# Kernel tuning notes

Hardware: AMD Instinct MI355X
Metric: run time of the kernel (lower is better)

## Reference

```python
import jax, jax.numpy as jnp
import numpy as np

B, S, D_IN, D_OUT, H = 4, 2048, 1024, 1024, 16
HD = D_OUT // H  # head_dim = 64


def setup_inputs() -> dict:
    key = jax.random.key(0)
    ks = jax.random.split(key, 9)
    sc_in = 1.0 / np.sqrt(D_IN)
    sc_out = 1.0 / np.sqrt(D_OUT)
    return {
        "x": jax.random.normal(ks[0], (B, S, D_IN), dtype=jnp.float32),
        "Wq": jax.random.normal(ks[1], (D_IN, D_OUT), dtype=jnp.float32) * sc_in,
        "bq": jax.random.normal(ks[2], (D_OUT,), dtype=jnp.float32) * 0.01,
        "Wk": jax.random.normal(ks[3], (D_IN, D_OUT), dtype=jnp.float32) * sc_in,
        "bk": jax.random.normal(ks[4], (D_OUT,), dtype=jnp.float32) * 0.01,
        "Wv": jax.random.normal(ks[5], (D_IN, D_OUT), dtype=jnp.float32) * sc_in,
        "bv": jax.random.normal(ks[6], (D_OUT,), dtype=jnp.float32) * 0.01,
        "Wo": jax.random.normal(ks[7], (D_OUT, D_OUT), dtype=jnp.float32) * sc_out,
        "bo": jax.random.normal(ks[8], (D_OUT,), dtype=jnp.float32) * 0.01,
    }


def reference(x, Wq, bq, Wk, bk, Wv, bv, Wo, bo):
    b, s, _ = x.shape
    # QKV projections -> [b, h, s, hd]
    def proj(W, bias):
        return (x @ W + bias).reshape(b, s, H, HD).transpose(0, 2, 1, 3)
    q, k, v = proj(Wq, bq), proj(Wk, bk), proj(Wv, bv)
    # scaled scores [b, h, s, s] with causal mask (future positions -> -inf)
    scores = jnp.einsum("bhqd,bhkd->bhqk", q, k) / jnp.sqrt(jnp.float32(HD))
    causal = jnp.triu(jnp.ones((s, s), dtype=bool), k=1)
    scores = jnp.where(causal, -jnp.inf, scores)
    attn = jax.nn.softmax(scores, axis=-1)  # dropout p=0.0 -> identity
    ctx = jnp.einsum("bhqk,bhkd->bhqd", attn, v)
    ctx = ctx.transpose(0, 2, 1, 3).reshape(b, s, D_OUT)
    return ctx @ Wo + bo
```

## Files before the change

### kernel.cpp

```cpp
#include <hip/hip_runtime.h>
#include <hip/hip_bf16.h>

#define B_   4
#define S_   2048
#define H_   16
#define HD_  64
#define D_   1024
#define M_   (B_ * S_)
#define N3_  3072

typedef unsigned short u16;
typedef __bf16 bf16x8 __attribute__((ext_vector_type(8)));
typedef float  f32x4  __attribute__((ext_vector_type(4)));
typedef int    i32x4  __attribute__((ext_vector_type(4)));
typedef unsigned short u16x8 __attribute__((ext_vector_type(8)));
typedef unsigned short u16x4 __attribute__((ext_vector_type(4)));

__device__ __forceinline__ float b2f(u16 u) {
    unsigned int x = ((unsigned int)u) << 16;
    return __builtin_bit_cast(float, x);
}
__device__ __forceinline__ u16 f2b(float f) {
    unsigned int x = __builtin_bit_cast(unsigned int, f);
    x += 0x7fffu + ((x >> 16) & 1u);
    return (u16)(x >> 16);
}

typedef const __attribute__((address_space(1))) unsigned int* gas_u32p;
typedef __attribute__((address_space(3))) unsigned int* las_u32p;
__device__ __forceinline__ void gl_lds16(const u16* g, u16* lds_base) {
    __builtin_amdgcn_global_load_lds((gas_u32p)g, (las_u32p)lds_base, 16, 0, 0);
}

__global__ __launch_bounds__(256) void cvt_k(const float* __restrict__ in,
                                             u16* __restrict__ out) {
    size_t i = ((size_t)blockIdx.x * 256 + threadIdx.x) * 8;
    float4 a = *(const float4*)(in + i);
    float4 b = *(const float4*)(in + i + 4);
    *(u16x8*)(out + i) = u16x8{f2b(a.x), f2b(a.y), f2b(a.z), f2b(a.w),
                               f2b(b.x), f2b(b.y), f2b(b.z), f2b(b.w)};
}

__global__ __launch_bounds__(256) void transpose4_k(
    const float* __restrict__ w0, const float* __restrict__ w1,
    const float* __restrict__ w2, const float* __restrict__ w3,
    u16* __restrict__ oqkv, u16* __restrict__ owo, float scale0) {
    __shared__ u16 t[32][33];
    const int z = blockIdx.z;
    const float* in = (z == 0) ? w0 : (z == 1) ? w1 : (z == 2) ? w2 : w3;
    u16* out = (z < 3) ? oqkv + (size_t)z * D_ * D_ : owo;
    const float sc = (z == 0) ? scale0 : 1.0f;
    const int x0 = blockIdx.x * 32, y0 = blockIdx.y * 32;
    const int tx = threadIdx.x & 31, ty = threadIdx.x >> 5;
#pragma unroll
    for (int i = 0; i < 32; i += 8)
        t[ty + i][tx] = f2b(in[(size_t)(y0 + ty + i) * D_ + x0 + tx] * sc);
    __syncthreads();
#pragma unroll
    for (int i = 0; i < 32; i += 8)
        out[(size_t)(x0 + ty + i) * D_ + y0 + tx] = t[tx][ty + i];
}

#define QBM 256
#define QBN 192
#define QBK 64

__global__ __launch_bounds__(512, 2) void gemm_qkv256(
    const u16* __restrict__ A, const u16* __restrict__ Bt,
    const float* __restrict__ b0, const float* __restrict__ b1,
    const float* __restrict__ b2, float cscale,
    u16* __restrict__ Qo, u16* __restrict__ Ko, u16* __restrict__ Vto,
    int M, int N, int K)
{
    __shared__ __align__(16) u16 As[2][QBM * QBK];
    __shared__ __align__(16) u16 Bs[2][QBN * QBK];

    const int tid  = threadIdx.x;
    const int lane = tid & 63;
    const int wave = tid >> 6;
    const int wr = wave >> 2, wc = wave & 3;
    const int l15 = lane & 15, quad = lane >> 4, s7 = l15 & 7;
    const int r8  = lane >> 3;
    const int csw = ((lane & 7) ^ r8) * 8;
    const int m0 = blockIdx.x * QBM, n0 = blockIdx.y * QBN;
    (void)M; (void)N;

    const u16* Ag = A  + (size_t)(m0 + wave * 8 + r8) * K + csw;
    const u16* Bg = Bt + (size_t)(n0 + wave * 8 + r8) * K + csw;
    u16* AsW = &As[0][0] + wave * 8 * QBK;
    u16* BsW = &Bs[0][0] + wave * 8 * QBK;
    const size_t rowK64 = (size_t)64 * K;

    auto stgA = [&](int buf, int u, int kt) {
        gl_lds16(Ag + (size_t)u * rowK64 + kt * QBK,
                 AsW + buf * (QBM * QBK) + u * 64 * QBK);
    };
    auto stgB = [&](int buf, int u, int kt) {
        gl_lds16(Bg + (size_t)u * rowK64 + kt * QBK,
                 BsW + buf * (QBN * QBK) + u * 64 * QBK);
    };

    f32x4 acc[8][3] = {};

    stgA(0, 0, 0); stgA(0, 1, 0); stgA(0, 2, 0); stgA(0, 3, 0);
    stgB(0, 0, 0); stgB(0, 1, 0); stgB(0, 2, 0);
    stgB(1, 0, 1); stgB(1, 1, 1); stgB(1, 2, 1);
    asm volatile("s_waitcnt vmcnt(3)" ::: "memory");
    __builtin_amdgcn_s_barrier();

    const int NIT = K / (2 * QBK);
    for (int it = 0; it < NIT; ++it) {
        const bool last = (it == NIT - 1);
        const int t1 = 2 * it + 1, t2 = 2 * it + 2, t3 = 2 * it + 3;
        bf16x8 bn[3][2];
#pragma unroll
        for (int ph = 0; ph < 4; ++ph) {
            const int hb = ph >> 1;
            const int qg = ph & 1;
            const u16* as = &As[hb][0];
            const u16* bs = &Bs[hb][0];
            if (qg == 0) {
#pragma unroll
                for (int n = 0; n < 3; ++n) {
                    const u16* bp = bs + (wc * 48 + n * 16 + l15) * QBK;
                    bn[n][0] = *(const bf16x8*)(bp + ((quad    ) ^ s7) * 8);
                    bn[n][1] = *(const bf16x8*)(bp + ((quad + 4) ^ s7) * 8);
                }
            }
            bf16x8 af[4][2];
#pragma unroll
            for (int r = 0; r < 4; ++r) {
                const u16* ap = as + (wr * 128 + (qg * 4 + r) * 16 + l15) * QBK;
                af[r][0] = *(const bf16x8*)(ap + ((quad    ) ^ s7) * 8);
                af[r][1] = *(const bf16x8*)(ap + ((quad + 4) ^ s7) * 8);
            }
            if (ph == 0) { stgA(1, 0, t1); stgA(1, 1, t1);
                           stgA(1, 2, t1); stgA(1, 3, t1); }
            if (!last) {
                if (ph == 1) { stgB(0, 0, t2); stgB(0, 1, t2); stgB(0, 2, t2); }
                if (ph == 2) { stgA(0, 0, t2); stgA(0, 1, t2);
                               stgA(0, 2, t2); stgA(0, 3, t2); }
                if (ph == 3) { stgB(1, 0, t3); stgB(1, 1, t3); stgB(1, 2, t3); }
            }
            __builtin_amdgcn_s_barrier();
            asm volatile("s_waitcnt lgkmcnt(0)" ::: "memory");
            __builtin_amdgcn_sched_barrier(0);
            __builtin_amdgcn_s_setprio(1);
#pragma unroll
            for (int r = 0; r < 4; ++r)
#pragma unroll
                for (int n = 0; n < 3; ++n) {
                    acc[qg * 4 + r][n] = __builtin_amdgcn_mfma_f32_16x16x32_bf16(
                        af[r][0], bn[n][0], acc[qg * 4 + r][n], 0, 0, 0);
                    acc[qg * 4 + r][n] = __builtin_amdgcn_mfma_f32_16x16x32_bf16(
                        af[r][1], bn[n][1], acc[qg * 4 + r][n], 0, 0, 0);
                }
            __builtin_amdgcn_s_setprio(0);
            if (ph == 1) {
                if (!last) asm volatile("s_waitcnt vmcnt(3)" ::: "memory");
                else       asm volatile("s_waitcnt vmcnt(0)" ::: "memory");
            }
            if (ph == 3 && !last)
                asm volatile("s_waitcnt vmcnt(3)" ::: "memory");
            __builtin_amdgcn_s_barrier();
        }
    }

    int qidxv[3]; int ncolv[3]; float bvv[3];
#pragma unroll
    for (int nt = 0; nt < 3; ++nt) {
        const int col = n0 + wc * 48 + nt * 16 + l15;
        qidxv[nt] = col >> 10;
        ncolv[nt] = col & (D_ - 1);
        bvv[nt] = (qidxv[nt] == 0) ? b0[ncolv[nt]] * cscale
                : (qidxv[nt] == 1) ? b1[ncolv[nt]] : b2[ncolv[nt]];
    }
#pragma unroll
    for (int mt = 0; mt < 8; ++mt) {
        const int rbase = m0 + wr * 128 + mt * 16 + quad * 4;
#pragma unroll
        for (int r2 = 0; r2 < 4; ++r2) {
#pragma unroll
            for (int nt = 0; nt < 3; ++nt) {
                if (qidxv[nt] == 2) continue;
                u16* dst = (qidxv[nt] == 0) ? Qo : Ko;
                dst[(size_t)(rbase + r2) * D_ + ncolv[nt]] =
                    f2b(acc[mt][nt][r2] + bvv[nt]);
            }
        }
#pragma unroll
        for (int nt = 0; nt < 3; ++nt) {
            if (qidxv[nt] != 2) continue;
            const int bidx = rbase >> 11, s = rbase & (S_ - 1);
            const int hh = ncolv[nt] >> 6, hd = ncolv[nt] & 63;
            u16x4 pk{f2b(acc[mt][nt][0] + bvv[nt]), f2b(acc[mt][nt][1] + bvv[nt]),
                     f2b(acc[mt][nt][2] + bvv[nt]), f2b(acc[mt][nt][3] + bvv[nt])};
            *(u16x4*)(Vto + (((size_t)(bidx * H_ + hh)) * HD_ + hd) * S_ + s) = pk;
        }
    }
}

#define BM 128
#define BN 128
#define BK 64

template <int MODE>
__global__ __launch_bounds__(256) void gemm_core(
    const u16* __restrict__ A, const u16* __restrict__ Bt,
    const float* __restrict__ b0, const float* __restrict__ b1,
    const float* __restrict__ b2, float cscale,
    void* __restrict__ O0, void* __restrict__ O1, void* __restrict__ O2,
    int M, int N, int K)
{
    __shared__ __align__(16) u16 As[BM * BK];
    __shared__ __align__(16) u16 Bs[BN * BK];

    const int tid  = threadIdx.x;
    const int lane = tid & 63;
    const int wave = tid >> 6;
    const int wr = wave >> 1, wc = wave & 1;
    const int l15 = lane & 15, quad = lane >> 4;
    const int m0 = blockIdx.x * BM, n0 = blockIdx.y * BN;
    const int r8 = lane >> 3;
    const int csw = ((lane & 7) ^ r8) * 8;

    f32x4 acc[4][4] = {};

    for (int k0 = 0; k0 < K; k0 += BK) {
#pragma unroll
        for (int i = 0; i < 4; ++i) {
            const int row = wave * 32 + i * 8 + r8;
            gl_lds16(A  + (size_t)(m0 + row) * K + k0 + csw,
                     As + (wave * 32 + i * 8) * BK);
            gl_lds16(Bt + (size_t)(n0 + row) * K + k0 + csw,
                     Bs + (wave * 32 + i * 8) * BK);
        }
        __syncthreads();
        bf16x8 af[4][2], bfr[4][2];
#pragma unroll
        for (int t = 0; t < 4; ++t) {
            const u16* ap = As + (wr * 64 + t * 16 + l15) * BK;
            const u16* bp = Bs + (wc * 64 + t * 16 + l15) * BK;
            const int s7 = l15 & 7;
            af[t][0]  = *(const bf16x8*)(ap + ((quad    ) ^ s7) * 8);
            af[t][1]  = *(const bf16x8*)(ap + ((quad + 4) ^ s7) * 8);
            bfr[t][0] = *(const bf16x8*)(bp + ((quad    ) ^ s7) * 8);
            bfr[t][1] = *(const bf16x8*)(bp + ((quad + 4) ^ s7) * 8);
        }
#pragma unroll
        for (int mt = 0; mt < 4; ++mt)
#pragma unroll
            for (int nt = 0; nt < 4; ++nt) {
                acc[mt][nt] = __builtin_amdgcn_mfma_f32_16x16x32_bf16(
                    af[mt][0], bfr[nt][0], acc[mt][nt], 0, 0, 0);
                acc[mt][nt] = __builtin_amdgcn_mfma_f32_16x16x32_bf16(
                    af[mt][1], bfr[nt][1], acc[mt][nt], 0, 0, 0);
            }
        __syncthreads();
    }

#pragma unroll
    for (int nt = 0; nt < 4; ++nt) {
        const int col = n0 + wc * 64 + nt * 16 + l15;
        if constexpr (MODE == 1) {
            const float bv = b0[col];
#pragma unroll
            for (int mt = 0; mt < 4; ++mt) {
                const int rbase = m0 + wr * 64 + mt * 16 + quad * 4;
#pragma unroll
                for (int r2 = 0; r2 < 4; ++r2)
                    ((float*)O0)[(size_t)(rbase + r2) * N + col] =
                        acc[mt][nt][r2] + bv;
            }
        } else {
            const int qidx = col >> 10, ncol = col & (D_ - 1);
            const float bv = (qidx == 0) ? b0[ncol] * cscale
                           : (qidx == 1) ? b1[ncol] : b2[ncol];
#pragma unroll
            for (int mt = 0; mt < 4; ++mt) {
                const int rbase = m0 + wr * 64 + mt * 16 + quad * 4;
                if (qidx == 2) {
                    const int bidx = rbase >> 11, s = rbase & (S_ - 1);
                    const int hh = ncol >> 6, hd = ncol & 63;
                    u16x4 pk{f2b(acc[mt][nt][0] + bv), f2b(acc[mt][nt][1] + bv),
                             f2b(acc[mt][nt][2] + bv), f2b(acc[mt][nt][3] + bv)};
                    *(u16x4*)((u16*)O2 +
                        (((size_t)(bidx * H_ + hh)) * HD_ + hd) * S_ + s) = pk;
                } else {
                    u16* dst = (qidx == 0) ? (u16*)O0 : (u16*)O1;
#pragma unroll
                    for (int r2 = 0; r2 < 4; ++r2)
                        dst[(size_t)(rbase + r2) * D_ + ncol] =
                            f2b(acc[mt][nt][r2] + bv);
                }
            }
        }
    }
}

__global__ __launch_bounds__(256, 4) void attn_mfma_k(
    const u16* __restrict__ Qm, const u16* __restrict__ Km,
    const u16* __restrict__ Vtg, u16* __restrict__ Om)
{
    __shared__ __align__(16) u16 Kbuf[2][64 * 64];
    __shared__ __align__(16) u16 Vbuf[2][64 * 64];
    __shared__ __align__(16) u16 Ps[4][16 * 64];

    const int tid  = threadIdx.x;
    const int lane = tid & 63;
    const int wave = tid >> 6;
    const int l15  = lane & 15;
    const int quad = lane >> 4;
    const int s7   = l15 & 7;
    const int bh = blockIdx.x, b = bh >> 4, h = bh & (H_ - 1);
    const int j  = blockIdx.y;
    const int dg0 = j, dg1 = 31 - j;

    const u16* Qg = Qm + (size_t)b * S_ * D_ + h * HD_;
    const u16* Kg = Km + (size_t)b * S_ * D_ + h * HD_;
    const u16* Vg = Vtg + ((size_t)(b * H_ + h)) * HD_ * S_;

    bf16x8 qf0[2], qf1[2];
    {
        const u16* qp = Qg + (size_t)(dg0 * 64 + wave * 16 + l15) * D_ + quad * 8;
        qf0[0] = *(const bf16x8*)qp; qf0[1] = *(const bf16x8*)(qp + 32);
        qp = Qg + (size_t)(dg1 * 64 + wave * 16 + l15) * D_ + quad * 8;
        qf1[0] = *(const bf16x8*)qp; qf1[1] = *(const bf16x8*)(qp + 32);
    }

    f32x4 of0[4] = {}, of1[4] = {};
    float lacc0 = 0.f, lacc1 = 0.f;
    const int qloc = wave * 16 + l15;
    const int r8 = lane >> 3;
    const int csw = ((lane & 7) ^ r8) * 8;
    const int srcA = l15 + ((quad & 1) << 5);
    const int srcB = srcA + 16;

    auto stage = [&](int t, int bsel) {
        u16* kb = Kbuf[bsel];
        u16* vb = Vbuf[bsel];
#pragma unroll
        for (int i = 0; i < 2; ++i) {
            const int row = wave * 16 + i * 8 + r8;
            gl_lds16(Kg + (size_t)(t * 64 + row) * D_ + csw,
                     kb + (wave * 16 + i * 8) * 64);
            gl_lds16(Vg + (size_t)row * S_ + t * 64 + csw,
                     vb + (wave * 16 + i * 8) * 64);
        }
    };

    auto pass = [&](const bf16x8 (&q)[2], f32x4 (&o)[4], float& la,
                    bool domask, const u16* kb, const u16* vb) {
        f32x4 sf[4];
#pragma unroll
        for (int kt = 0; kt < 4; ++kt) {
            const u16* kp = kb + (kt * 16 + l15) * 64;
            bf16x8 k0 = *(const bf16x8*)(kp + ((quad    ) ^ s7) * 8);
            bf16x8 k1 = *(const bf16x8*)(kp + ((quad + 4) ^ s7) * 8);
            f32x4 a = {};
            a = __builtin_amdgcn_mfma_f32_16x16x32_bf16(k0, q[0], a, 0, 0, 0);
            a = __builtin_amdgcn_mfma_f32_16x16x32_bf16(k1, q[1], a, 0, 0, 0);
            sf[kt] = a;
        }
        unsigned int w[4][2];
        float ls = 0.f;
        if (domask) {
#pragma unroll
            for (int kt = 0; kt < 4; ++kt)
#pragma unroll
                for (int hh = 0; hh < 2; ++hh) {
                    float v0 = sf[kt][2 * hh], v1 = sf[kt][2 * hh + 1];
                    if (kt * 16 + quad * 4 + 2 * hh     > qloc) v0 = -INFINITY;
                    if (kt * 16 + quad * 4 + 2 * hh + 1 > qloc) v1 = -INFINITY;
                    float p0 = __builtin_amdgcn_exp2f(v0);
                    float p1 = __builtin_amdgcn_exp2f(v1);
                    ls += p0 + p1;
                    w[kt][hh] = (__builtin_bit_cast(unsigned int, p0) >> 16) |
                                (__builtin_bit_cast(unsigned int, p1) & 0xFFFF0000u);
                }
        } else {
#pragma unroll
            for (int kt = 0; kt < 4; ++kt)
#pragma unroll
                for (int hh = 0; hh < 2; ++hh) {
                    float p0 = __builtin_amdgcn_exp2f(sf[kt][2 * hh]);
                    float p1 = __builtin_amdgcn_exp2f(sf[kt][2 * hh + 1]);
                    ls += p0 + p1;
                    w[kt][hh] = (__builtin_bit_cast(unsigned int, p0) >> 16) |
                                (__builtin_bit_cast(unsigned int, p1) & 0xFFFF0000u);
                }
        }
        la += ls;
        const bool hi = (quad & 2) != 0;
        i32x4 f0, f1;
        {
            int a0, a1;
            a0 = __shfl((int)w[0][0], srcA); a1 = __shfl((int)w[1][0], srcA);
            f0.x = hi ? a1 : a0;
            a0 = __shfl((int)w[0][1], srcA); a1 = __shfl((int)w[1][1], srcA);
            f0.y = hi ? a1 : a0;
            a0 = __shfl((int)w[0][0], srcB); a1 = __shfl((int)w[1][0], srcB);
            f0.z = hi ? a1 : a0;
            a0 = __shfl((int)w[0][1], srcB); a1 = __shfl((int)w[1][1], srcB);
            f0.w = hi ? a1 : a0;
            a0 = __shfl((int)w[2][0], srcA); a1 = __shfl((int)w[3][0], srcA);
            f1.x = hi ? a1 : a0;
            a0 = __shfl((int)w[2][1], srcA); a1 = __shfl((int)w[3][1], srcA);
            f1.y = hi ? a1 : a0;
            a0 = __shfl((int)w[2][0], srcB); a1 = __shfl((int)w[3][0], srcB);
            f1.z = hi ? a1 : a0;
            a0 = __shfl((int)w[2][1], srcB); a1 = __shfl((int)w[3][1], srcB);
            f1.w = hi ? a1 : a0;
        }
        bf16x8 pf0 = __builtin_bit_cast(bf16x8, f0);
        bf16x8 pf1 = __builtin_bit_cast(bf16x8, f1);
#pragma unroll
        for (int dt = 0; dt < 4; ++dt) {
            const u16* vp = vb + (dt * 16 + l15) * 64;
            bf16x8 v0 = *(const bf16x8*)(vp + ((quad    ) ^ s7) * 8);
            bf16x8 v1 = *(const bf16x8*)(vp + ((quad + 4) ^ s7) * 8);
            o[dt] = __builtin_amdgcn_mfma_f32_16x16x32_bf16(v0, pf0, o[dt], 0, 0, 0);
            o[dt] = __builtin_amdgcn_mfma_f32_16x16x32_bf16(v1, pf1, o[dt], 0, 0, 0);
        }
    };

    const int T = 32 - j;
    stage(0, 0);
    for (int t = 0; t < T; ++t) {
        __syncthreads();
        if (t + 1 < T) stage(t + 1, (t + 1) & 1);
        const u16* kb = Kbuf[t & 1];
        const u16* vb = Vbuf[t & 1];
        if (t <= dg0) pass(qf0, of0, lacc0, t == dg0, kb, vb);
        pass(qf1, of1, lacc1, t == dg1, kb, vb);
    }

    u16* pw = Ps[wave];
    auto epi = [&](const f32x4 (&o)[4], float la, int dgq) {
        float ls = la;
        ls += __shfl_xor(ls, 16);
        ls += __shfl_xor(ls, 32);
        const float inv = 1.f / ls;
#pragma unroll
        for (int dt = 0; dt < 4; ++dt) {
            const int g = dt * 16 + quad * 4;
            const int pos = ((g >> 3) ^ s7) * 8 + (g & 7);
            *(u16x4*)(pw + l15 * 64 + pos) =
                u16x4{f2b(o[dt][0] * inv), f2b(o[dt][1] * inv),
                      f2b(o[dt][2] * inv), f2b(o[dt][3] * inv)};
        }
        const int r  = lane >> 2;
        const int cp = lane & 3;
        u16x8 o0 = *(const u16x8*)(pw + r * 64 + ((2 * cp    ) ^ (r & 7)) * 8);
        u16x8 o1 = *(const u16x8*)(pw + r * 64 + ((2 * cp + 1) ^ (r & 7)) * 8);
        u16* op = Om + ((size_t)(b * S_ + dgq * 64 + wave * 16 + r)) * D_ + h * 64 + cp * 16;
        *(u16x8*)op = o0;
        *(u16x8*)(op + 8) = o1;
    };
    epi(of0, lacc0, dg0);
    epi(of1, lacc1, dg1);
}

extern "C" void kernel_launch(void* const* d_in, const int* in_sizes, int n_in,
                              void* d_out, int out_size, void* d_ws, size_t ws_size,
                              hipStream_t stream)
{
    (void)in_sizes; (void)n_in; (void)out_size; (void)ws_size;
    const float* x  = (const float*)d_in[0];
    const float* Wq = (const float*)d_in[1];
    const float* bq = (const float*)d_in[2];
    const float* Wk = (const float*)d_in[3];
    const float* bk = (const float*)d_in[4];
    const float* Wv = (const float*)d_in[5];
    const float* bv = (const float*)d_in[6];
    const float* Wo = (const float*)d_in[7];
    const float* bo = (const float*)d_in[8];

    const float cscale = 0.18033688011112042f;

    u16* ws = (u16*)d_ws;
    const size_t MD = (size_t)M_ * D_;
    const size_t DD = (size_t)D_ * D_;
    u16* xb    = ws;
    u16* Qb    = xb + MD;
    u16* Kb    = Qb + MD;
    u16* Vtb   = Kb + MD;
    u16* Cb    = Vtb + MD;
    u16* WqkvT = Cb + MD;
    u16* WoT   = WqkvT + 3 * DD;

    cvt_k<<<M_ * D_ / 2048, 256, 0, stream>>>(x, xb);

    transpose4_k<<<dim3(D_ / 32, D_ / 32, 4), 256, 0, stream>>>(
        Wq, Wk, Wv, Wo, WqkvT, WoT, cscale);

    gemm_qkv256<<<dim3(M_ / QBM, N3_ / QBN), 512, 0, stream>>>(
        xb, WqkvT, bq, bk, bv, cscale, Qb, Kb, Vtb, M_, N3_, D_);

    attn_mfma_k<<<dim3(B_ * H_, 16), 256, 0, stream>>>(Qb, Kb, Vtb, Cb);

    gemm_core<1><<<dim3(M_ / BM, D_ / BN), 256, 0, stream>>>(
        Cb, WoT, bo, nullptr, nullptr, 1.0f, d_out, nullptr, nullptr, M_, D_, D_);
}
```

Before: 264.8 us.

## Interleave both query tiles' QK and PV MFMAs sharing K/V LDS loads, add setprio

Splits the per-tile attention pass into score, softmax and PV phases and runs the two query fragments together, so each K and V fragment read from LDS feeds MFMAs for both query tiles. Interleaving independent MFMA chains is meant to hide MFMA latency and halve LDS reads for K/V. s_setprio raises wave priority around the MFMA phases to encourage overlap with other waves' softmax. This raises register pressure by holding two score sets live at once.

```diff
diff --git a/kernel.cpp b/kernel.cpp
--- a/kernel.cpp
+++ b/kernel.cpp
@@ -349,19 +349,8 @@
         }
     };
 
-    auto pass = [&](const bf16x8 (&q)[2], f32x4 (&o)[4], float& la,
-                    bool domask, const u16* kb, const u16* vb) {
-        f32x4 sf[4];
-#pragma unroll
-        for (int kt = 0; kt < 4; ++kt) {
-            const u16* kp = kb + (kt * 16 + l15) * 64;
-            bf16x8 k0 = *(const bf16x8*)(kp + ((quad    ) ^ s7) * 8);
-            bf16x8 k1 = *(const bf16x8*)(kp + ((quad + 4) ^ s7) * 8);
-            f32x4 a = {};
-            a = __builtin_amdgcn_mfma_f32_16x16x32_bf16(k0, q[0], a, 0, 0, 0);
-            a = __builtin_amdgcn_mfma_f32_16x16x32_bf16(k1, q[1], a, 0, 0, 0);
-            sf[kt] = a;
-        }
+    auto smax = [&](const f32x4 (&sf)[4], bool domask, float& la,
+                    bf16x8& pfa, bf16x8& pfb) {
         unsigned int w[4][2];
         float ls = 0.f;
         if (domask) {
@@ -412,16 +401,8 @@
             a0 = __shfl((int)w[2][1], srcB); a1 = __shfl((int)w[3][1], srcB);
             f1.w = hi ? a1 : a0;
         }
-        bf16x8 pf0 = __builtin_bit_cast(bf16x8, f0);
-        bf16x8 pf1 = __builtin_bit_cast(bf16x8, f1);
-#pragma unroll
-        for (int dt = 0; dt < 4; ++dt) {
-            const u16* vp = vb + (dt * 16 + l15) * 64;
-            bf16x8 v0 = *(const bf16x8*)(vp + ((quad    ) ^ s7) * 8);
-            bf16x8 v1 = *(const bf16x8*)(vp + ((quad + 4) ^ s7) * 8);
-            o[dt] = __builtin_amdgcn_mfma_f32_16x16x32_bf16(v0, pf0, o[dt], 0, 0, 0);
-            o[dt] = __builtin_amdgcn_mfma_f32_16x16x32_bf16(v1, pf1, o[dt], 0, 0, 0);
-        }
+        pfa = __builtin_bit_cast(bf16x8, f0);
+        pfb = __builtin_bit_cast(bf16x8, f1);
     };
 
     const int T = 32 - j;
@@ -431,8 +412,67 @@
         if (t + 1 < T) stage(t + 1, (t + 1) & 1);
         const u16* kb = Kbuf[t & 1];
         const u16* vb = Vbuf[t & 1];
-        if (t <= dg0) pass(qf0, of0, lacc0, t == dg0, kb, vb);
-        pass(qf1, of1, lacc1, t == dg1, kb, vb);
+
+        if (t <= dg0) {
+            f32x4 s0[4], s1[4];
+            __builtin_amdgcn_s_setprio(1);
+#pragma unroll
+            for (int kt = 0; kt < 4; ++kt) {
+                const u16* kp = kb + (kt * 16 + l15) * 64;
+                bf16x8 k0 = *(const bf16x8*)(kp + ((quad    ) ^ s7) * 8);
+                bf16x8 k1 = *(const bf16x8*)(kp + ((quad + 4) ^ s7) * 8);
+                f32x4 a = {};
+                a = __builtin_amdgcn_mfma_f32_16x16x32_bf16(k0, qf0[0], a, 0, 0, 0);
+                a = __builtin_amdgcn_mfma_f32_16x16x32_bf16(k1, qf0[1], a, 0, 0, 0);
+                s0[kt] = a;
+                f32x4 c = {};
+                c = __builtin_amdgcn_mfma_f32_16x16x32_bf16(k0, qf1[0], c, 0, 0, 0);
+                c = __builtin_amdgcn_mfma_f32_16x16x32_bf16(k1, qf1[1], c, 0, 0, 0);
+                s1[kt] = c;
+            }
+            __builtin_amdgcn_s_setprio(0);
+            bf16x8 p00, p01, p10, p11;
+            smax(s0, t == dg0, lacc0, p00, p01);
+            smax(s1, false,    lacc1, p10, p11);
+            __builtin_amdgcn_s_setprio(1);
+#pragma unroll
+            for (int dt = 0; dt < 4; ++dt) {
+                const u16* vp = vb + (dt * 16 + l15) * 64;
+                bf16x8 v0 = *(const bf16x8*)(vp + ((quad    ) ^ s7) * 8);
+                bf16x8 v1 = *(const bf16x8*)(vp + ((quad + 4) ^ s7) * 8);
+                of0[dt] = __builtin_amdgcn_mfma_f32_16x16x32_bf16(v0, p00, of0[dt], 0, 0, 0);
+                of0[dt] = __builtin_amdgcn_mfma_f32_16x16x32_bf16(v1, p01, of0[dt], 0, 0, 0);
+                of1[dt] = __builtin_amdgcn_mfma_f32_16x16x32_bf16(v0, p10, of1[dt], 0, 0, 0);
+                of1[dt] = __builtin_amdgcn_mfma_f32_16x16x32_bf16(v1, p11, of1[dt], 0, 0, 0);
+            }
+            __builtin_amdgcn_s_setprio(0);
+        } else {
+            f32x4 s1[4];
+            __builtin_amdgcn_s_setprio(1);
+#pragma unroll
+            for (int kt = 0; kt < 4; ++kt) {
+                const u16* kp = kb + (kt * 16 + l15) * 64;
+                bf16x8 k0 = *(const bf16x8*)(kp + ((quad    ) ^ s7) * 8);
+                bf16x8 k1 = *(const bf16x8*)(kp + ((quad + 4) ^ s7) * 8);
+                f32x4 c = {};
+                c = __builtin_amdgcn_mfma_f32_16x16x32_bf16(k0, qf1[0], c, 0, 0, 0);
+                c = __builtin_amdgcn_mfma_f32_16x16x32_bf16(k1, qf1[1], c, 0, 0, 0);
+                s1[kt] = c;
+            }
+            __builtin_amdgcn_s_setprio(0);
+            bf16x8 p10, p11;
+            smax(s1, t == dg1, lacc1, p10, p11);
+            __builtin_amdgcn_s_setprio(1);
+#pragma unroll
+            for (int dt = 0; dt < 4; ++dt) {
+                const u16* vp = vb + (dt * 16 + l15) * 64;
+                bf16x8 v0 = *(const bf16x8*)(vp + ((quad    ) ^ s7) * 8);
+                bf16x8 v1 = *(const bf16x8*)(vp + ((quad + 4) ^ s7) * 8);
+                of1[dt] = __builtin_amdgcn_mfma_f32_16x16x32_bf16(v0, p10, of1[dt], 0, 0, 0);
+                of1[dt] = __builtin_amdgcn_mfma_f32_16x16x32_bf16(v1, p11, of1[dt], 0, 0, 0);
+            }
+            __builtin_amdgcn_s_setprio(0);
+        }
     }
 
     u16* pw = Ps[wave];
```

After: 284.3 us. 1.07x slower.

## Read K and V tiles directly from global memory instead of LDS staging

Applied to the files above, without the earlier changes.

Drops the double-buffered global-to-LDS staging of K and V tiles, along with the per-iteration __syncthreads, in the causal attention kernel. Each wave now loads its MFMA operands straight from global memory, relying on L1/L2 caching across the four waves that read the same tile. This removes the barriers and the LDS traffic, but it multiplies global and cache load requests by the wave count and loses the prefetch overlap. Any latency hiding now depends on the compiler's scheduling and on occupancy.

```diff
diff --git a/kernel.cpp b/kernel.cpp
--- a/kernel.cpp
+++ b/kernel.cpp
@@ -302,8 +302,6 @@
     const u16* __restrict__ Qm, const u16* __restrict__ Km,
     const u16* __restrict__ Vtg, u16* __restrict__ Om)
 {
-    __shared__ __align__(16) u16 Kbuf[2][64 * 64];
-    __shared__ __align__(16) u16 Vbuf[2][64 * 64];
     __shared__ __align__(16) u16 Ps[4][16 * 64];
 
     const int tid  = threadIdx.x;
@@ -331,32 +329,18 @@
     f32x4 of0[4] = {}, of1[4] = {};
     float lacc0 = 0.f, lacc1 = 0.f;
     const int qloc = wave * 16 + l15;
-    const int r8 = lane >> 3;
-    const int csw = ((lane & 7) ^ r8) * 8;
     const int srcA = l15 + ((quad & 1) << 5);
     const int srcB = srcA + 16;
 
-    auto stage = [&](int t, int bsel) {
-        u16* kb = Kbuf[bsel];
-        u16* vb = Vbuf[bsel];
-#pragma unroll
-        for (int i = 0; i < 2; ++i) {
-            const int row = wave * 16 + i * 8 + r8;
-            gl_lds16(Kg + (size_t)(t * 64 + row) * D_ + csw,
-                     kb + (wave * 16 + i * 8) * 64);
-            gl_lds16(Vg + (size_t)row * S_ + t * 64 + csw,
-                     vb + (wave * 16 + i * 8) * 64);
-        }
-    };
-
     auto pass = [&](const bf16x8 (&q)[2], f32x4 (&o)[4], float& la,
-                    bool domask, const u16* kb, const u16* vb) {
+                    bool domask, int t) {
         f32x4 sf[4];
+        const u16* kp0 = Kg + (size_t)(t * 64 + l15) * D_ + quad * 8;
 #pragma unroll
         for (int kt = 0; kt < 4; ++kt) {
-            const u16* kp = kb + (kt * 16 + l15) * 64;
-            bf16x8 k0 = *(const bf16x8*)(kp + ((quad    ) ^ s7) * 8);
-            bf16x8 k1 = *(const bf16x8*)(kp + ((quad + 4) ^ s7) * 8);
+            const u16* kp = kp0 + (size_t)(kt * 16) * D_;
+            bf16x8 k0 = *(const bf16x8*)kp;
+            bf16x8 k1 = *(const bf16x8*)(kp + 32);
             f32x4 a = {};
             a = __builtin_amdgcn_mfma_f32_16x16x32_bf16(k0, q[0], a, 0, 0, 0);
             a = __builtin_amdgcn_mfma_f32_16x16x32_bf16(k1, q[1], a, 0, 0, 0);
@@ -416,23 +400,18 @@
         bf16x8 pf1 = __builtin_bit_cast(bf16x8, f1);
 #pragma unroll
         for (int dt = 0; dt < 4; ++dt) {
-            const u16* vp = vb + (dt * 16 + l15) * 64;
-            bf16x8 v0 = *(const bf16x8*)(vp + ((quad    ) ^ s7) * 8);
-            bf16x8 v1 = *(const bf16x8*)(vp + ((quad + 4) ^ s7) * 8);
+            const u16* vp = Vg + (size_t)(dt * 16 + l15) * S_ + t * 64 + quad * 8;
+            bf16x8 v0 = *(const bf16x8*)vp;
+            bf16x8 v1 = *(const bf16x8*)(vp + 32);
             o[dt] = __builtin_amdgcn_mfma_f32_16x16x32_bf16(v0, pf0, o[dt], 0, 0, 0);
             o[dt] = __builtin_amdgcn_mfma_f32_16x16x32_bf16(v1, pf1, o[dt], 0, 0, 0);
         }
     };
 
     const int T = 32 - j;
-    stage(0, 0);
     for (int t = 0; t < T; ++t) {
-        __syncthreads();
-        if (t + 1 < T) stage(t + 1, (t + 1) & 1);
-        const u16* kb = Kbuf[t & 1];
-        const u16* vb = Vbuf[t & 1];
-        if (t <= dg0) pass(qf0, of0, lacc0, t == dg0, kb, vb);
-        pass(qf1, of1, lacc1, t == dg1, kb, vb);
+        if (t <= dg0) pass(qf0, of0, lacc0, t == dg0, t);
+        pass(qf1, of1, lacc1, t == dg1, t);
     }
 
     u16* pw = Ps[wave];
```

Result: slower. 438.0 us (+65.4%).
